# Kernel tuning notes

Hardware: AMD Instinct MI355X
Metric: run time of the kernel (lower is better)

Reference implementation:

```python
import jax, jax.numpy as jnp
import numpy as np

DIM = 192
HEADS = 4
EMBED = 48


def setup_inputs() -> dict:
    key = jax.random.key(0)
    ks = jax.random.split(key, 8)
    b, c, h, w = 8, DIM, 128, 128
    x = jax.random.normal(ks[0], (b, c, h, w), dtype=jnp.float32)
    prior = jax.random.normal(ks[1], (b, 1, EMBED * 4), dtype=jnp.float32)
    # learned params (bias=False)
    w_qkv = jax.random.normal(ks[2], (3 * c, c), dtype=jnp.float32) * (1.0 / np.sqrt(c))
    w_dw = jax.random.normal(ks[3], (3 * c, 1, 3, 3), dtype=jnp.float32) * (1.0 / 3.0)
    w_proj = jax.random.normal(ks[4], (c, c), dtype=jnp.float32) * (1.0 / np.sqrt(c))
    w_kernel = jax.random.normal(ks[5], (2 * c, EMBED * 4), dtype=jnp.float32) * (1.0 / np.sqrt(EMBED * 4))
    temperature = jnp.ones((HEADS, 1, 1), dtype=jnp.float32)
    return {"x": x, "prior": prior, "w_qkv": w_qkv, "w_dw": w_dw,
            "w_proj": w_proj, "w_kernel": w_kernel, "temperature": temperature}


def _mdta(x, prior, w_qkv, w_dw, w_proj, w_kernel, temperature):
    b, c, h, w = x.shape
    # prior modulation: Linear(4*embed -> 2*dim), broadcast over (h,w)
    kv = jnp.einsum('blf,of->blo', prior, w_kernel)[:, 0]        # (b, 2c)
    kv1, kv2 = kv[:, :c], kv[:, c:]
    x = x * kv1[:, :, None, None] + kv2[:, :, None, None]
    # 1x1 conv -> depthwise 3x3 conv
    qkv = jnp.einsum('bchw,oc->bohw', x, w_qkv)                   # (b, 3c, h, w)
    qkv = jax.lax.conv_general_dilated(
        qkv, w_dw, window_strides=(1, 1), padding='SAME',
        dimension_numbers=('NCHW', 'OIHW', 'NCHW'), feature_group_count=3 * c)
    q, k, v = jnp.split(qkv, 3, axis=1)
    ch = c // HEADS
    def heads(t):  # (b, c, h, w) -> (b, head, ch, h*w)
        return t.reshape(b, HEADS, ch, h * w)
    q, k, v = heads(q), heads(k), heads(v)
    # L2 normalize over the (h w) reduction axis
    q = q / jnp.linalg.norm(q, axis=-1, keepdims=True).clip(1e-12)
    k = k / jnp.linalg.norm(k, axis=-1, keepdims=True).clip(1e-12)
    attn = jnp.einsum('bhcn,bhdn->bhcd', q, k) * temperature      # (b, head, ch, ch)
    attn = jax.nn.softmax(attn, axis=-1)
    out = jnp.einsum('bhcd,bhdn->bhcn', attn, v).reshape(b, c, h, w)
    return jnp.einsum('bchw,oc->bohw', out, w_proj)


def reference(x, prior, w_qkv, w_dw, w_proj, w_kernel, temperature):
    return _mdta(x, prior, w_qkv, w_dw, w_proj, w_kernel, temperature)
```

## Files before the change

### kernel.cpp

```cpp
#include <hip/hip_runtime.h>
#include <hip/hip_bf16.h>
#include <stdint.h>

typedef float f32x4 __attribute__((ext_vector_type(4)));
typedef __bf16 bf16x8 __attribute__((ext_vector_type(8)));
typedef __bf16 bf16x2 __attribute__((ext_vector_type(2)));

#define NB 8
#define NC 192
#define NO 576
#define NH 128
#define NWID 128
#define NSP 16384
#define NHEADS 4
#define NCH 48

#define OFF_KV    0u
#define OFF_SSQ   12288u
#define OFF_S     24576u
#define OFF_WB    319488u
#define OFF_M     540672u
#define OFF_XT    1130496u
#define OFF_QKV1  152125440u

__device__ __forceinline__ void g2l16(const void* g, void* l) {
    __builtin_amdgcn_global_load_lds((const __attribute__((address_space(1))) void*)g,
                                     (__attribute__((address_space(3))) void*)l, 16, 0, 0);
}

__global__ void k_kv(const float* __restrict__ prior, const float* __restrict__ w_kernel,
                     float* __restrict__ kv) {
    int t = blockIdx.x * 256 + threadIdx.x;
    if (t >= NB * 384) return;
    int b = t / 384, j = t % 384;
    const float* p = prior + b * NC;
    const float* wk = w_kernel + j * NC;
    float s = 0.f;
    for (int f = 0; f < NC; ++f) s += p[f] * wk[f];
    kv[t] = s;
}

__global__ void k_wcast(const float* __restrict__ w_qkv, __bf16* __restrict__ Wb) {
    int t = blockIdx.x * 256 + threadIdx.x;
    if (t < NO * NC) Wb[t] = (__bf16)w_qkv[t];
}

__global__ __launch_bounds__(256) void k_xt(const float* __restrict__ x, const float* __restrict__ kv,
                                            __bf16* __restrict__ xt) {
    int b = blockIdx.y;
    int n0 = blockIdx.x * 128;
    __shared__ __align__(16) __bf16 lds[128 * 192];
    int t = threadIdx.x;
    for (int p = 0; p < 24; ++p) {
        int id = p * 256 + t;
        int c = id >> 5, n4 = (id & 31) << 2;
        f32x4 v = *reinterpret_cast<const f32x4*>(x + (size_t)(b * NC + c) * NSP + n0 + n4);
        float k1 = kv[b * 384 + c], k2 = kv[b * 384 + 192 + c];
        int chi = (c >> 3) ^ ((n4 >> 2) & 7);
        int base = chi * 16 + (c & 7) * 2;
#pragma unroll
        for (int j = 0; j < 4; ++j)
            *reinterpret_cast<__bf16*>((char*)lds + (n4 + j) * 384 + base) = (__bf16)(v[j] * k1 + k2);
    }
    __syncthreads();
    for (int p = 0; p < 12; ++p) {
        int id = p * 256 + t;
        int n = id / 24, k = id % 24;
        bf16x8 r = *reinterpret_cast<const bf16x8*>((char*)lds + n * 384 + ((k ^ ((n >> 2) & 7)) << 4));
        *reinterpret_cast<bf16x8*>(xt + (size_t)(b * NSP + n0 + n) * NC + k * 8) = r;
    }
}

__global__ __launch_bounds__(256, 2) void k_qkv(const __bf16* __restrict__ xt, const __bf16* __restrict__ Wb,
                                                __bf16* __restrict__ qkv1) {
    __shared__ __align__(16) char lds[73728];
    int b = blockIdx.y, n0 = blockIdx.x * 128;
    int t = threadIdx.x;
    const __bf16* bsrc = xt + (size_t)(b * NSP + n0) * NC;
#pragma unroll
    for (int i = 0; i < 12; ++i) {
        int s = i * 256 + t;
        int r = s / 24, c = s % 24, g = c ^ (r & 7);
        g2l16(bsrc + (size_t)r * NC + g * 8, lds + s * 16);
    }
#pragma unroll
    for (int i = 0; i < 6; ++i) {
        int s = i * 256 + t;
        int r = s / 24, c = s % 24, g = c ^ (r & 7);
        g2l16(Wb + (size_t)r * NC + g * 8, lds + 49152 + s * 16);
    }
    asm volatile("s_waitcnt vmcnt(0)" ::: "memory");
    __syncthreads();
    int w = t >> 6, l = t & 63, lr = l & 15, lg = l >> 4;
    bf16x8 bgf[6][2];
#pragma unroll
    for (int ks = 0; ks < 6; ++ks) {
        int c16 = ks * 4 + lg;
#pragma unroll
        for (int nf = 0; nf < 2; ++nf) {
            int r = w * 32 + nf * 16 + lr;
            bgf[ks][nf] = *reinterpret_cast<const bf16x8*>(lds + r * 384 + ((c16 ^ (r & 7)) << 4));
        }
    }
    for (int ot = 0; ot < 9; ++ot) {
        f32x4 acc[4][2] = {};
#pragma unroll
        for (int ks = 0; ks < 6; ++ks) {
            int c16 = ks * 4 + lg;
            bf16x8 a[4];
#pragma unroll
            for (int mf = 0; mf < 4; ++mf) {
                int r = mf * 16 + lr;
                a[mf] = *reinterpret_cast<const bf16x8*>(lds + 49152 + r * 384 + ((c16 ^ (r & 7)) << 4));
            }
#pragma unroll
            for (int mf = 0; mf < 4; ++mf)
#pragma unroll
                for (int nf = 0; nf < 2; ++nf)
                    acc[mf][nf] = __builtin_amdgcn_mfma_f32_16x16x32_bf16(a[mf], bgf[ks][nf], acc[mf][nf], 0, 0, 0);
        }
        __syncthreads();
        if (ot < 8) {
            const __bf16* asrc = Wb + (size_t)(ot + 1) * 64 * NC;
#pragma unroll
            for (int i = 0; i < 6; ++i) {
                int s = i * 256 + t;
                int r = s / 24, c = s % 24, g = c ^ (r & 7);
                g2l16(asrc + (size_t)r * NC + g * 8, lds + 49152 + s * 16);
            }
        }
        int o0 = ot * 64;
#pragma unroll
        for (int mf = 0; mf < 4; ++mf)
#pragma unroll
            for (int rr = 0; rr < 4; ++rr) {
                int orow = o0 + mf * 16 + lg * 4 + rr;
#pragma unroll
                for (int nf = 0; nf < 2; ++nf)
                    qkv1[(size_t)(b * NO + orow) * NSP + n0 + w * 32 + nf * 16 + lr] = (__bf16)acc[mf][nf][rr];
            }
        if (ot < 8) {
            asm volatile("s_waitcnt vmcnt(32)" ::: "memory");
            __syncthreads();
        }
    }
}

__global__ __launch_bounds__(256) void k_dw(const __bf16* __restrict__ qkv1, const float* __restrict__ w_dw,
                                            __bf16* __restrict__ qkv2, float* __restrict__ ssq) {
    int task = blockIdx.x * 4 + (threadIdx.x >> 6);
    int l = threadIdx.x & 63;
    int strip = task & 7;
    int bo = task >> 3;
    int o = bo % NO, b = bo / NO;
    const __bf16* src = qkv1 + (size_t)bo * NSP;
    __bf16* dst = qkv2 + (size_t)bo * NSP;
    float wd[9];
#pragma unroll
    for (int i = 0; i < 9; ++i) wd[i] = w_dw[o * 9 + i];
    int ys = strip * 16;
    float a0, b0, L0, R0, a1, b1, L1, R1, a2, b2, L2, R2;

#define LOADROW(Y, A, B, L_, R_) {                                            \
        bf16x2 p = {};                                                        \
        int y_ = (Y);                                                         \
        if (y_ >= 0 && y_ < NH) p = *reinterpret_cast<const bf16x2*>(src + y_ * NWID + 2 * l); \
        A = (float)p[0]; B = (float)p[1];                                     \
        L_ = __shfl(B, l - 1); R_ = __shfl(A, l + 1);                         \
        if (l == 0) L_ = 0.f;                                                 \
        if (l == 63) R_ = 0.f; }

    LOADROW(ys - 1, a0, b0, L0, R0)
    LOADROW(ys,     a1, b1, L1, R1)
    float ss = 0.f;
    bool qk = (o < 384);
#pragma unroll 4
    for (int i = 0; i < 16; ++i) {
        LOADROW(ys + i + 1, a2, b2, L2, R2)
        float oa = L0 * wd[0] + a0 * wd[1] + b0 * wd[2]
                 + L1 * wd[3] + a1 * wd[4] + b1 * wd[5]
                 + L2 * wd[6] + a2 * wd[7] + b2 * wd[8];
        float ob = a0 * wd[0] + b0 * wd[1] + R0 * wd[2]
                 + a1 * wd[3] + b1 * wd[4] + R1 * wd[5]
                 + a2 * wd[6] + b2 * wd[7] + R2 * wd[8];
        bf16x2 ov; ov[0] = (__bf16)oa; ov[1] = (__bf16)ob;
        *reinterpret_cast<bf16x2*>(dst + (ys + i) * NWID + 2 * l) = ov;
        if (qk) { float fa = (float)ov[0], fb = (float)ov[1]; ss += fa * fa + fb * fb; }
        a0 = a1; b0 = b1; L0 = L1; R0 = R1;
        a1 = a2; b1 = b2; L1 = L2; R1 = R2;
    }
#undef LOADROW
    if (qk) {
        for (int off = 32; off > 0; off >>= 1) ss += __shfl_down(ss, off);
        if (l == 0) atomicAdd(&ssq[b * 384 + o], ss);
    }
}

__global__ __launch_bounds__(256) void k_vt(const __bf16* __restrict__ qkv2, __bf16* __restrict__ vt) {
    int b = blockIdx.y;
    int n0 = blockIdx.x * 128;
    __shared__ __align__(16) __bf16 lds[128 * 192];
    int t = threadIdx.x;
    for (int p = 0; p < 12; ++p) {
        int id = p * 256 + t;
        int c = id >> 4, n8 = (id & 15) << 3;
        bf16x8 v = *reinterpret_cast<const bf16x8*>(qkv2 + (size_t)(b * NO + 384 + c) * NSP + n0 + n8);
        int chi = (c >> 3) ^ ((n8 >> 3) & 7);
        int base = chi * 16 + (c & 7) * 2;
#pragma unroll
        for (int j = 0; j < 8; ++j)
            *reinterpret_cast<__bf16*>((char*)lds + (n8 + j) * 384 + base) = v[j];
    }
    __syncthreads();
    for (int p = 0; p < 12; ++p) {
        int id = p * 256 + t;
        int n = id / 24, k = id % 24;
        bf16x8 r = *reinterpret_cast<const bf16x8*>((char*)lds + n * 384 + ((k ^ ((n >> 3) & 7)) << 4));
        *reinterpret_cast<bf16x8*>(vt + (size_t)(b * NSP + n0 + n) * NC + k * 8) = r;
    }
}

__global__ __launch_bounds__(256, 3) void k_sdot(const __bf16* __restrict__ qkv2, float* __restrict__ S) {
    __shared__ __align__(16) char lds[49152];
    int b = blockIdx.z, h = blockIdx.y, n0 = blockIdx.x * 512;
    int t = threadIdx.x;
    int w = t >> 6, l = t & 63, lr = l & 15, lg = l >> 4;
    const __bf16* qsrc = qkv2 + (size_t)(b * NO + h * NCH) * NSP + n0;
    const __bf16* ksrc = qkv2 + (size_t)(b * NO + 192 + h * NCH) * NSP + n0;
    f32x4 acc[3][3] = {};
    for (int pass = 0; pass < 2; ++pass) {
        if (pass) __syncthreads();
        int coff = pass * 256;
#pragma unroll
        for (int i = 0; i < 6; ++i) {
            int s = i * 256 + t;
            int r = s >> 5, c = s & 31, g = c ^ (r & 7);
            g2l16(qsrc + (size_t)r * NSP + coff + g * 8, lds + s * 16);
        }
#pragma unroll
        for (int i = 0; i < 6; ++i) {
            int s = i * 256 + t;
            int r = s >> 5, c = s & 31, g = c ^ (r & 7);
            g2l16(ksrc + (size_t)r * NSP + coff + g * 8, lds + 24576 + s * 16);
        }
        asm volatile("s_waitcnt vmcnt(0)" ::: "memory");
        __syncthreads();
#pragma unroll
        for (int j = 0; j < 2; ++j) {
            int c16 = (w * 2 + j) * 4 + lg;
            bf16x8 a[3], bb[3];
#pragma unroll
            for (int mf = 0; mf < 3; ++mf) {
                int r = mf * 16 + lr;
                a[mf] = *reinterpret_cast<const bf16x8*>(lds + r * 512 + ((c16 ^ (r & 7)) << 4));
            }
#pragma unroll
            for (int nf = 0; nf < 3; ++nf) {
                int r = nf * 16 + lr;
                bb[nf] = *reinterpret_cast<const bf16x8*>(lds + 24576 + r * 512 + ((c16 ^ (r & 7)) << 4));
            }
#pragma unroll
            for (int mf = 0; mf < 3; ++mf)
#pragma unroll
                for (int nf = 0; nf < 3; ++nf)
                    acc[mf][nf] = __builtin_amdgcn_mfma_f32_16x16x32_bf16(a[mf], bb[nf], acc[mf][nf], 0, 0, 0);
        }
    }
    __syncthreads();
    float* red = (float*)lds;
#pragma unroll
    for (int mf = 0; mf < 3; ++mf)
#pragma unroll
        for (int nf = 0; nf < 3; ++nf)
#pragma unroll
            for (int r = 0; r < 4; ++r) {
                int c = mf * 16 + lg * 4 + r, d = nf * 16 + lr;
                red[(w * 48 + c) * 49 + d] = acc[mf][nf][r];
            }
    __syncthreads();
    float* Sb = S + (size_t)(b * NHEADS + h) * NCH * NCH;
    for (int i = 0; i < 9; ++i) {
        int idx = t + i * 256;
        int c = idx / 48, d = idx % 48;
        float s = red[c * 49 + d] + red[(48 + c) * 49 + d] + red[(96 + c) * 49 + d] + red[(144 + c) * 49 + d];
        atomicAdd(&Sb[c * 48 + d], s);
    }
}

__global__ __launch_bounds__(256) void k_soft(const float* __restrict__ S, const float* __restrict__ ssq,
                                              const float* __restrict__ temp, const float* __restrict__ w_proj,
                                              __bf16* __restrict__ M) {
    int b = blockIdx.x / NHEADS, h = blockIdx.x % NHEADS;
    int tid = threadIdx.x;
    __shared__ float attn[48][48];
    __shared__ float inv[96];
    if (tid < 96) {
        int c = tid % 48;
        int isK = tid / 48;
        float v = ssq[b * 384 + isK * 192 + h * NCH + c];
        float nrm = fmaxf(sqrtf(v), 1e-12f);
        inv[tid] = 1.f / nrm;
    }
    __syncthreads();
    float tp = temp[h];
    const float* Sb = S + (size_t)(b * NHEADS + h) * NCH * NCH;
    for (int i = 0; i < 9; ++i) {
        int idx = tid + i * 256;
        int c = idx / 48, d = idx % 48;
        attn[c][d] = Sb[c * 48 + d] * inv[c] * inv[48 + d] * tp;
    }
    __syncthreads();
    if (tid < 48) {
        float m = -1e30f;
        for (int d = 0; d < 48; ++d) m = fmaxf(m, attn[tid][d]);
        float sum = 0.f;
        for (int d = 0; d < 48; ++d) { float e = __expf(attn[tid][d] - m); attn[tid][d] = e; sum += e; }
        float r = 1.f / sum;
        for (int d = 0; d < 48; ++d) attn[tid][d] *= r;
    }
    __syncthreads();
    for (int i = 0; i < 36; ++i) {
        int idx = tid + i * 256;
        int oo = idx / 48, d = idx % 48;
        const float* wp = w_proj + oo * NC + h * NCH;
        float s = 0.f;
        for (int c = 0; c < 48; ++c) s += wp[c] * attn[c][d];
        M[(size_t)(b * NC + oo) * NC + h * NCH + d] = (__bf16)s;
    }
}

__global__ __launch_bounds__(256, 2) void k_out(const __bf16* __restrict__ Mw, const __bf16* __restrict__ vt,
                                                float* __restrict__ outp) {
    __shared__ __align__(16) char lds[73728];
    int b = blockIdx.y, n0 = blockIdx.x * 128;
    int t = threadIdx.x;
    const __bf16* bsrc = vt + (size_t)(b * NSP + n0) * NC;
#pragma unroll
    for (int i = 0; i < 12; ++i) {
        int s = i * 256 + t;
        int r = s / 24, c = s % 24, g = c ^ (r & 7);
        g2l16(bsrc + (size_t)r * NC + g * 8, lds + s * 16);
    }
    const __bf16* asrc0 = Mw + (size_t)(b * NC) * NC;
#pragma unroll
    for (int i = 0; i < 6; ++i) {
        int s = i * 256 + t;
        int r = s / 24, c = s % 24, g = c ^ (r & 7);
        g2l16(asrc0 + (size_t)r * NC + g * 8, lds + 49152 + s * 16);
    }
    asm volatile("s_waitcnt vmcnt(0)" ::: "memory");
    __syncthreads();
    int w = t >> 6, l = t & 63, lr = l & 15, lg = l >> 4;
    bf16x8 bgf[6][2];
#pragma unroll
    for (int ks = 0; ks < 6; ++ks) {
        int c16 = ks * 4 + lg;
#pragma unroll
        for (int nf = 0; nf < 2; ++nf) {
            int r = w * 32 + nf * 16 + lr;
            bgf[ks][nf] = *reinterpret_cast<const bf16x8*>(lds + r * 384 + ((c16 ^ (r & 7)) << 4));
        }
    }
    for (int ot = 0; ot < 3; ++ot) {
        f32x4 acc[4][2] = {};
#pragma unroll
        for (int ks = 0; ks < 6; ++ks) {
            int c16 = ks * 4 + lg;
            bf16x8 a[4];
#pragma unroll
            for (int mf = 0; mf < 4; ++mf) {
                int r = mf * 16 + lr;
                a[mf] = *reinterpret_cast<const bf16x8*>(lds + 49152 + r * 384 + ((c16 ^ (r & 7)) << 4));
            }
#pragma unroll
            for (int mf = 0; mf < 4; ++mf)
#pragma unroll
                for (int nf = 0; nf < 2; ++nf)
                    acc[mf][nf] = __builtin_amdgcn_mfma_f32_16x16x32_bf16(a[mf], bgf[ks][nf], acc[mf][nf], 0, 0, 0);
        }
        __syncthreads();
        if (ot < 2) {
            const __bf16* asrc = Mw + (size_t)(b * NC + (ot + 1) * 64) * NC;
#pragma unroll
            for (int i = 0; i < 6; ++i) {
                int s = i * 256 + t;
                int r = s / 24, c = s % 24, g = c ^ (r & 7);
                g2l16(asrc + (size_t)r * NC + g * 8, lds + 49152 + s * 16);
            }
        }
        int o0 = ot * 64;
#pragma unroll
        for (int mf = 0; mf < 4; ++mf)
#pragma unroll
            for (int rr = 0; rr < 4; ++rr) {
                int orow = o0 + mf * 16 + lg * 4 + rr;
#pragma unroll
                for (int nf = 0; nf < 2; ++nf)
                    outp[(size_t)(b * NC + orow) * NSP + n0 + w * 32 + nf * 16 + lr] = acc[mf][nf][rr];
            }
        if (ot < 2) {
            asm volatile("s_waitcnt vmcnt(32)" ::: "memory");
            __syncthreads();
        }
    }
}

extern "C" void kernel_launch(void* const* d_in, const int* in_sizes, int n_in,
                              void* d_out, int out_size, void* d_ws, size_t ws_size,
                              hipStream_t stream) {
    const float* x        = (const float*)d_in[0];
    const float* prior    = (const float*)d_in[1];
    const float* w_qkv    = (const float*)d_in[2];
    const float* w_dw     = (const float*)d_in[3];
    const float* w_proj   = (const float*)d_in[4];
    const float* w_kernel = (const float*)d_in[5];
    const float* temp     = (const float*)d_in[6];
    char* ws = (char*)d_ws;
    float*  kv    = (float*)(ws + OFF_KV);
    float*  ssq   = (float*)(ws + OFF_SSQ);
    float*  S     = (float*)(ws + OFF_S);
    __bf16* Wb    = (__bf16*)(ws + OFF_WB);
    __bf16* M     = (__bf16*)(ws + OFF_M);
    __bf16* xt    = (__bf16*)(ws + OFF_XT);
    __bf16* qkv2  = (__bf16*)(ws + OFF_XT);
    __bf16* qkv1  = (__bf16*)(ws + OFF_QKV1);
    __bf16* vt    = (__bf16*)(ws + OFF_QKV1);
    float*  outp  = (float*)d_out;

    hipMemsetAsync(ws + OFF_SSQ, 0, 12288 + 294912, stream);

    k_kv<<<12, 256, 0, stream>>>(prior, w_kernel, kv);
    k_wcast<<<432, 256, 0, stream>>>(w_qkv, Wb);
    k_xt<<<dim3(128, 8), 256, 0, stream>>>(x, kv, xt);
    k_qkv<<<dim3(128, 8), 256, 0, stream>>>(xt, Wb, qkv1);
    k_dw<<<9216, 256, 0, stream>>>(qkv1, w_dw, qkv2, ssq);
    k_vt<<<dim3(128, 8), 256, 0, stream>>>(qkv2, vt);
    k_sdot<<<dim3(32, 4, 8), 256, 0, stream>>>(qkv2, S);
    k_soft<<<32, 256, 0, stream>>>(S, ssq, temp, w_proj, M);
    k_out<<<dim3(128, 8), 256, 0, stream>>>(M, vt, outp);
}
```

Baseline: 251.7 us.

## Fuse input modulation/transpose into QKV GEMM and V transpose into output GEMM

Removes the separate k_xt and k_vt transpose kernels by having k_qkv read fp32 x directly, apply the prior modulation, convert to bf16 and write it transposed into LDS. k_out likewise gathers V from the channel-major qkv2 buffer into swizzled LDS. The memset is folded into k_kv as a zeroing loop. This avoids two full intermediate tensor round trips through global memory and two launches, at the cost of strided per-element global loads (stride NSP) inside the GEMM kernels.

```diff
diff --git a/kernel.cpp b/kernel.cpp
--- a/kernel.cpp
+++ b/kernel.cpp
@@ -20,7 +20,7 @@
 #define OFF_S     24576u
 #define OFF_WB    319488u
 #define OFF_M     540672u
-#define OFF_XT    1130496u
+#define OFF_QKV2  1130496u
 #define OFF_QKV1  152125440u
 
 __device__ __forceinline__ void g2l16(const void* g, void* l) {
@@ -29,8 +29,9 @@
 }
 
 __global__ void k_kv(const float* __restrict__ prior, const float* __restrict__ w_kernel,
-                     float* __restrict__ kv) {
+                     float* __restrict__ kv, float* __restrict__ zbase) {
     int t = blockIdx.x * 256 + threadIdx.x;
+    for (int i = t; i < 76800; i += 3072) zbase[i] = 0.f;
     if (t >= NB * 384) return;
     int b = t / 384, j = t % 384;
     const float* p = prior + b * NC;
@@ -45,49 +46,31 @@
     if (t < NO * NC) Wb[t] = (__bf16)w_qkv[t];
 }
 
-__global__ __launch_bounds__(256) void k_xt(const float* __restrict__ x, const float* __restrict__ kv,
-                                            __bf16* __restrict__ xt) {
-    int b = blockIdx.y;
-    int n0 = blockIdx.x * 128;
-    __shared__ __align__(16) __bf16 lds[128 * 192];
-    int t = threadIdx.x;
-    for (int p = 0; p < 24; ++p) {
-        int id = p * 256 + t;
-        int c = id >> 5, n4 = (id & 31) << 2;
-        f32x4 v = *reinterpret_cast<const f32x4*>(x + (size_t)(b * NC + c) * NSP + n0 + n4);
-        float k1 = kv[b * 384 + c], k2 = kv[b * 384 + 192 + c];
-        int chi = (c >> 3) ^ ((n4 >> 2) & 7);
-        int base = chi * 16 + (c & 7) * 2;
-#pragma unroll
-        for (int j = 0; j < 4; ++j)
-            *reinterpret_cast<__bf16*>((char*)lds + (n4 + j) * 384 + base) = (__bf16)(v[j] * k1 + k2);
-    }
-    __syncthreads();
-    for (int p = 0; p < 12; ++p) {
-        int id = p * 256 + t;
-        int n = id / 24, k = id % 24;
-        bf16x8 r = *reinterpret_cast<const bf16x8*>((char*)lds + n * 384 + ((k ^ ((n >> 2) & 7)) << 4));
-        *reinterpret_cast<bf16x8*>(xt + (size_t)(b * NSP + n0 + n) * NC + k * 8) = r;
-    }
-}
-
-__global__ __launch_bounds__(256, 2) void k_qkv(const __bf16* __restrict__ xt, const __bf16* __restrict__ Wb,
-                                                __bf16* __restrict__ qkv1) {
+__global__ __launch_bounds__(256, 2) void k_qkv(const float* __restrict__ x, const float* __restrict__ kv,
+                                                const __bf16* __restrict__ Wb, __bf16* __restrict__ qkv1) {
     __shared__ __align__(16) char lds[73728];
     int b = blockIdx.y, n0 = blockIdx.x * 128;
     int t = threadIdx.x;
-    const __bf16* bsrc = xt + (size_t)(b * NSP + n0) * NC;
-#pragma unroll
-    for (int i = 0; i < 12; ++i) {
-        int s = i * 256 + t;
-        int r = s / 24, c = s % 24, g = c ^ (r & 7);
-        g2l16(bsrc + (size_t)r * NC + g * 8, lds + s * 16);
-    }
 #pragma unroll
     for (int i = 0; i < 6; ++i) {
         int s = i * 256 + t;
         int r = s / 24, c = s % 24, g = c ^ (r & 7);
         g2l16(Wb + (size_t)r * NC + g * 8, lds + 49152 + s * 16);
+    }
+    const float* xb = x + (size_t)b * NC * NSP + n0;
+    const float* kvb = kv + b * 384;
+#pragma unroll 4
+    for (int p = 0; p < 12; ++p) {
+        int task = p * 256 + t;
+        int n = task & 127, ch = task >> 7;
+        bf16x8 vv;
+#pragma unroll
+        for (int j = 0; j < 8; ++j) {
+            int c = ch * 8 + j;
+            float xv = xb[(size_t)c * NSP + n];
+            vv[j] = (__bf16)(xv * kvb[c] + kvb[192 + c]);
+        }
+        *reinterpret_cast<bf16x8*>(lds + n * 384 + ((ch ^ (n & 7)) << 4)) = vv;
     }
     asm volatile("s_waitcnt vmcnt(0)" ::: "memory");
     __syncthreads();
@@ -196,30 +179,6 @@
     }
 }
 
-__global__ __launch_bounds__(256) void k_vt(const __bf16* __restrict__ qkv2, __bf16* __restrict__ vt) {
-    int b = blockIdx.y;
-    int n0 = blockIdx.x * 128;
-    __shared__ __align__(16) __bf16 lds[128 * 192];
-    int t = threadIdx.x;
-    for (int p = 0; p < 12; ++p) {
-        int id = p * 256 + t;
-        int c = id >> 4, n8 = (id & 15) << 3;
-        bf16x8 v = *reinterpret_cast<const bf16x8*>(qkv2 + (size_t)(b * NO + 384 + c) * NSP + n0 + n8);
-        int chi = (c >> 3) ^ ((n8 >> 3) & 7);
-        int base = chi * 16 + (c & 7) * 2;
-#pragma unroll
-        for (int j = 0; j < 8; ++j)
-            *reinterpret_cast<__bf16*>((char*)lds + (n8 + j) * 384 + base) = v[j];
-    }
-    __syncthreads();
-    for (int p = 0; p < 12; ++p) {
-        int id = p * 256 + t;
-        int n = id / 24, k = id % 24;
-        bf16x8 r = *reinterpret_cast<const bf16x8*>((char*)lds + n * 384 + ((k ^ ((n >> 3) & 7)) << 4));
-        *reinterpret_cast<bf16x8*>(vt + (size_t)(b * NSP + n0 + n) * NC + k * 8) = r;
-    }
-}
-
 __global__ __launch_bounds__(256, 3) void k_sdot(const __bf16* __restrict__ qkv2, float* __restrict__ S) {
     __shared__ __align__(16) char lds[49152];
     int b = blockIdx.z, h = blockIdx.y, n0 = blockIdx.x * 512;
@@ -329,24 +288,28 @@
     }
 }
 
-__global__ __launch_bounds__(256, 2) void k_out(const __bf16* __restrict__ Mw, const __bf16* __restrict__ vt,
+__global__ __launch_bounds__(256, 2) void k_out(const __bf16* __restrict__ Mw, const __bf16* __restrict__ qkv2,
                                                 float* __restrict__ outp) {
     __shared__ __align__(16) char lds[73728];
     int b = blockIdx.y, n0 = blockIdx.x * 128;
     int t = threadIdx.x;
-    const __bf16* bsrc = vt + (size_t)(b * NSP + n0) * NC;
-#pragma unroll
-    for (int i = 0; i < 12; ++i) {
-        int s = i * 256 + t;
-        int r = s / 24, c = s % 24, g = c ^ (r & 7);
-        g2l16(bsrc + (size_t)r * NC + g * 8, lds + s * 16);
-    }
     const __bf16* asrc0 = Mw + (size_t)(b * NC) * NC;
 #pragma unroll
     for (int i = 0; i < 6; ++i) {
         int s = i * 256 + t;
         int r = s / 24, c = s % 24, g = c ^ (r & 7);
         g2l16(asrc0 + (size_t)r * NC + g * 8, lds + 49152 + s * 16);
+    }
+    const __bf16* vb = qkv2 + (size_t)(b * NO + 384) * NSP + n0;
+#pragma unroll 4
+    for (int p = 0; p < 12; ++p) {
+        int task = p * 256 + t;
+        int n = task & 127, ch = task >> 7;
+        bf16x8 vv;
+#pragma unroll
+        for (int j = 0; j < 8; ++j)
+            vv[j] = vb[(size_t)(ch * 8 + j) * NSP + n];
+        *reinterpret_cast<bf16x8*>(lds + n * 384 + ((ch ^ (n & 7)) << 4)) = vv;
     }
     asm volatile("s_waitcnt vmcnt(0)" ::: "memory");
     __syncthreads();
@@ -421,21 +384,15 @@
     float*  S     = (float*)(ws + OFF_S);
     __bf16* Wb    = (__bf16*)(ws + OFF_WB);
     __bf16* M     = (__bf16*)(ws + OFF_M);
-    __bf16* xt    = (__bf16*)(ws + OFF_XT);
-    __bf16* qkv2  = (__bf16*)(ws + OFF_XT);
+    __bf16* qkv2  = (__bf16*)(ws + OFF_QKV2);
     __bf16* qkv1  = (__bf16*)(ws + OFF_QKV1);
-    __bf16* vt    = (__bf16*)(ws + OFF_QKV1);
     float*  outp  = (float*)d_out;
 
-    hipMemsetAsync(ws + OFF_SSQ, 0, 12288 + 294912, stream);
-
-    k_kv<<<12, 256, 0, stream>>>(prior, w_kernel, kv);
+    k_kv<<<12, 256, 0, stream>>>(prior, w_kernel, kv, (float*)(ws + OFF_SSQ));
     k_wcast<<<432, 256, 0, stream>>>(w_qkv, Wb);
-    k_xt<<<dim3(128, 8), 256, 0, stream>>>(x, kv, xt);
-    k_qkv<<<dim3(128, 8), 256, 0, stream>>>(xt, Wb, qkv1);
+    k_qkv<<<dim3(128, 8), 256, 0, stream>>>(x, kv, Wb, qkv1);
     k_dw<<<9216, 256, 0, stream>>>(qkv1, w_dw, qkv2, ssq);
-    k_vt<<<dim3(128, 8), 256, 0, stream>>>(qkv2, vt);
     k_sdot<<<dim3(32, 4, 8), 256, 0, stream>>>(qkv2, S);
     k_soft<<<32, 256, 0, stream>>>(S, ssq, temp, w_proj, M);
-    k_out<<<dim3(128, 8), 256, 0, stream>>>(M, vt, outp);
-}
+    k_out<<<dim3(128, 8), 256, 0, stream>>>(M, qkv2, outp);
+}
```

New measurement: 235.6 us. 1.07x faster.

## Fuse V transpose into output GEMM and merge prep kernels with memset

Applied to the files above, without the earlier changes.

Removes the separate k_vt transpose kernel: k_out now reads V directly from qkv2 in channel-major layout and transposes it into LDS while loading, using a new swizzle GR(r) to limit bank conflicts. The kv, weight-cast and workspace-zeroing steps are merged into one k_prep launch, replacing a memset and two kernels. This cuts a full write and re-read of V and several launches. The cost is slower scalar LDS stores and non-async loads in k_out, which no longer overlap with the M loads the way global_load_lds did.

```diff
diff --git a/kernel.cpp b/kernel.cpp
--- a/kernel.cpp
+++ b/kernel.cpp
@@ -4,6 +4,7 @@
 
 typedef float f32x4 __attribute__((ext_vector_type(4)));
 typedef __bf16 bf16x8 __attribute__((ext_vector_type(8)));
+typedef __bf16 bf16x4 __attribute__((ext_vector_type(4)));
 typedef __bf16 bf16x2 __attribute__((ext_vector_type(2)));
 
 #define NB 8
@@ -23,26 +24,27 @@
 #define OFF_XT    1130496u
 #define OFF_QKV1  152125440u
 
+#define GR(r) (((r) ^ ((r) >> 2)) & 7)
+
 __device__ __forceinline__ void g2l16(const void* g, void* l) {
     __builtin_amdgcn_global_load_lds((const __attribute__((address_space(1))) void*)g,
                                      (__attribute__((address_space(3))) void*)l, 16, 0, 0);
 }
 
-__global__ void k_kv(const float* __restrict__ prior, const float* __restrict__ w_kernel,
-                     float* __restrict__ kv) {
+__global__ void k_prep(const float* __restrict__ prior, const float* __restrict__ w_kernel,
+                       const float* __restrict__ w_qkv, float* __restrict__ kv,
+                       float* __restrict__ zbase, __bf16* __restrict__ Wb) {
     int t = blockIdx.x * 256 + threadIdx.x;
-    if (t >= NB * 384) return;
-    int b = t / 384, j = t % 384;
-    const float* p = prior + b * NC;
-    const float* wk = w_kernel + j * NC;
-    float s = 0.f;
-    for (int f = 0; f < NC; ++f) s += p[f] * wk[f];
-    kv[t] = s;
-}
-
-__global__ void k_wcast(const float* __restrict__ w_qkv, __bf16* __restrict__ Wb) {
-    int t = blockIdx.x * 256 + threadIdx.x;
+    if (t < 76800) zbase[t] = 0.f;
     if (t < NO * NC) Wb[t] = (__bf16)w_qkv[t];
+    if (t < NB * 384) {
+        int b = t / 384, j = t % 384;
+        const float* p = prior + b * NC;
+        const float* wk = w_kernel + j * NC;
+        float s = 0.f;
+        for (int f = 0; f < NC; ++f) s += p[f] * wk[f];
+        kv[t] = s;
+    }
 }
 
 __global__ __launch_bounds__(256) void k_xt(const float* __restrict__ x, const float* __restrict__ kv,
@@ -196,30 +198,6 @@
     }
 }
 
-__global__ __launch_bounds__(256) void k_vt(const __bf16* __restrict__ qkv2, __bf16* __restrict__ vt) {
-    int b = blockIdx.y;
-    int n0 = blockIdx.x * 128;
-    __shared__ __align__(16) __bf16 lds[128 * 192];
-    int t = threadIdx.x;
-    for (int p = 0; p < 12; ++p) {
-        int id = p * 256 + t;
-        int c = id >> 4, n8 = (id & 15) << 3;
-        bf16x8 v = *reinterpret_cast<const bf16x8*>(qkv2 + (size_t)(b * NO + 384 + c) * NSP + n0 + n8);
-        int chi = (c >> 3) ^ ((n8 >> 3) & 7);
-        int base = chi * 16 + (c & 7) * 2;
-#pragma unroll
-        for (int j = 0; j < 8; ++j)
-            *reinterpret_cast<__bf16*>((char*)lds + (n8 + j) * 384 + base) = v[j];
-    }
-    __syncthreads();
-    for (int p = 0; p < 12; ++p) {
-        int id = p * 256 + t;
-        int n = id / 24, k = id % 24;
-        bf16x8 r = *reinterpret_cast<const bf16x8*>((char*)lds + n * 384 + ((k ^ ((n >> 3) & 7)) << 4));
-        *reinterpret_cast<bf16x8*>(vt + (size_t)(b * NSP + n0 + n) * NC + k * 8) = r;
-    }
-}
-
 __global__ __launch_bounds__(256, 3) void k_sdot(const __bf16* __restrict__ qkv2, float* __restrict__ S) {
     __shared__ __align__(16) char lds[49152];
     int b = blockIdx.z, h = blockIdx.y, n0 = blockIdx.x * 512;
@@ -329,24 +307,30 @@
     }
 }
 
-__global__ __launch_bounds__(256, 2) void k_out(const __bf16* __restrict__ Mw, const __bf16* __restrict__ vt,
+__global__ __launch_bounds__(256, 2) void k_out(const __bf16* __restrict__ Mw, const __bf16* __restrict__ qkv2,
                                                 float* __restrict__ outp) {
     __shared__ __align__(16) char lds[73728];
     int b = blockIdx.y, n0 = blockIdx.x * 128;
     int t = threadIdx.x;
-    const __bf16* bsrc = vt + (size_t)(b * NSP + n0) * NC;
-#pragma unroll
-    for (int i = 0; i < 12; ++i) {
-        int s = i * 256 + t;
-        int r = s / 24, c = s % 24, g = c ^ (r & 7);
-        g2l16(bsrc + (size_t)r * NC + g * 8, lds + s * 16);
-    }
     const __bf16* asrc0 = Mw + (size_t)(b * NC) * NC;
 #pragma unroll
     for (int i = 0; i < 6; ++i) {
         int s = i * 256 + t;
-        int r = s / 24, c = s % 24, g = c ^ (r & 7);
+        int r = s / 24, c = s % 24, g = c ^ GR(r);
         g2l16(asrc0 + (size_t)r * NC + g * 8, lds + 49152 + s * 16);
+    }
+    const __bf16* vb = qkv2 + (size_t)(b * NO + 384) * NSP + n0;
+#pragma unroll 4
+    for (int p = 0; p < 24; ++p) {
+        int id = p * 256 + t;
+        int c = id >> 5, n4 = (id & 31) << 2;
+        bf16x4 vv = *reinterpret_cast<const bf16x4*>(vb + (size_t)c * NSP + n4);
+#pragma unroll
+        for (int j = 0; j < 4; ++j) {
+            int n = n4 + j;
+            int chi = (c >> 3) ^ GR(n);
+            *reinterpret_cast<__bf16*>((char*)lds + n * 384 + chi * 16 + (c & 7) * 2) = vv[j];
+        }
     }
     asm volatile("s_waitcnt vmcnt(0)" ::: "memory");
     __syncthreads();
@@ -358,7 +342,7 @@
 #pragma unroll
         for (int nf = 0; nf < 2; ++nf) {
             int r = w * 32 + nf * 16 + lr;
-            bgf[ks][nf] = *reinterpret_cast<const bf16x8*>(lds + r * 384 + ((c16 ^ (r & 7)) << 4));
+            bgf[ks][nf] = *reinterpret_cast<const bf16x8*>(lds + r * 384 + ((c16 ^ GR(r)) << 4));
         }
     }
     for (int ot = 0; ot < 3; ++ot) {
@@ -370,7 +354,7 @@
 #pragma unroll
             for (int mf = 0; mf < 4; ++mf) {
                 int r = mf * 16 + lr;
-                a[mf] = *reinterpret_cast<const bf16x8*>(lds + 49152 + r * 384 + ((c16 ^ (r & 7)) << 4));
+                a[mf] = *reinterpret_cast<const bf16x8*>(lds + 49152 + r * 384 + ((c16 ^ GR(r)) << 4));
             }
 #pragma unroll
             for (int mf = 0; mf < 4; ++mf)
@@ -384,7 +368,7 @@
 #pragma unroll
             for (int i = 0; i < 6; ++i) {
                 int s = i * 256 + t;
-                int r = s / 24, c = s % 24, g = c ^ (r & 7);
+                int r = s / 24, c = s % 24, g = c ^ GR(r);
                 g2l16(asrc + (size_t)r * NC + g * 8, lds + 49152 + s * 16);
             }
         }
@@ -424,18 +408,13 @@
     __bf16* xt    = (__bf16*)(ws + OFF_XT);
     __bf16* qkv2  = (__bf16*)(ws + OFF_XT);
     __bf16* qkv1  = (__bf16*)(ws + OFF_QKV1);
-    __bf16* vt    = (__bf16*)(ws + OFF_QKV1);
     float*  outp  = (float*)d_out;
 
-    hipMemsetAsync(ws + OFF_SSQ, 0, 12288 + 294912, stream);
-
-    k_kv<<<12, 256, 0, stream>>>(prior, w_kernel, kv);
-    k_wcast<<<432, 256, 0, stream>>>(w_qkv, Wb);
+    k_prep<<<432, 256, 0, stream>>>(prior, w_kernel, w_qkv, kv, (float*)(ws + OFF_SSQ), Wb);
     k_xt<<<dim3(128, 8), 256, 0, stream>>>(x, kv, xt);
     k_qkv<<<dim3(128, 8), 256, 0, stream>>>(xt, Wb, qkv1);
     k_dw<<<9216, 256, 0, stream>>>(qkv1, w_dw, qkv2, ssq);
-    k_vt<<<dim3(128, 8), 256, 0, stream>>>(qkv2, vt);
     k_sdot<<<dim3(32, 4, 8), 256, 0, stream>>>(qkv2, S);
     k_soft<<<32, 256, 0, stream>>>(S, ssq, temp, w_proj, M);
-    k_out<<<dim3(128, 8), 256, 0, stream>>>(M, vt, outp);
-}
+    k_out<<<dim3(128, 8), 256, 0, stream>>>(M, qkv2, outp);
+}
```

New measurement: 225.4 us. -10.5%, faster.
